# Kernel optimization log

Hardware: AMD Instinct MI355X
Metric: run time of the kernel (lower is better)

## Reference

```python
import jax, jax.numpy as jnp
import numpy as np

B, N, OUTERDIM, DIM, N_CLASSES = 2, 6000, 1024, 512, 2
HEADS, DIM_HEAD, INNER = 8, 64, 512
LANDMARKS, PINV_ITERS, KPAD = 256, 6, 16  # residual conv kernel 33 -> pad 16
SCALE = DIM_HEAD ** -0.5


def layer_norm(x, g, b, eps=1e-5):
    mu = x.mean(-1, keepdims=True)
    var = jnp.var(x, axis=-1, keepdims=True)
    return (x - mu) * jax.lax.rsqrt(var + eps) * g + b


def moore_penrose_pinv(x, iters=PINV_ITERS):
    # x: [b, h, m, m]
    abs_x = jnp.abs(x)
    col = abs_x.sum(-1)
    row = abs_x.sum(-2)
    z = jnp.swapaxes(x, -1, -2) / (jnp.max(col) * jnp.max(row))
    I = jnp.eye(x.shape[-1], dtype=x.dtype)
    for _ in range(iters):
        xz = x @ z
        z = 0.25 * z @ (13 * I - xz @ (15 * I - xz @ (7 * I - xz)))
    return z


def nystrom_attention(x, w_qkv, w_out, b_out, conv_w):
    b, n, _ = x.shape
    pad = (-n) % LANDMARKS
    xp = jnp.pad(x, ((0, 0), (pad, 0), (0, 0)))  # pad at FRONT, as in lucidrains impl
    npad = n + pad
    qkv = xp @ w_qkv.T  # [b, npad, 3*inner]
    q, k, v = [t.reshape(b, npad, HEADS, DIM_HEAD).transpose(0, 2, 1, 3)
               for t in jnp.split(qkv, 3, axis=-1)]
    q = q * SCALE
    l = npad // LANDMARKS  # tokens per landmark
    q_l = q.reshape(b, HEADS, LANDMARKS, l, DIM_HEAD).sum(3) / l
    k_l = k.reshape(b, HEADS, LANDMARKS, l, DIM_HEAD).sum(3) / l
    attn1 = jax.nn.softmax(jnp.einsum('bhid,bhjd->bhij', q, k_l), axis=-1)   # [b,h,npad,m]
    attn2 = jax.nn.softmax(jnp.einsum('bhid,bhjd->bhij', q_l, k_l), axis=-1)  # [b,h,m,m]
    attn3 = jax.nn.softmax(jnp.einsum('bhid,bhjd->bhij', q_l, k), axis=-1)    # [b,h,m,npad]
    out = (attn1 @ moore_penrose_pinv(attn2)) @ (attn3 @ v)  # [b,h,npad,d]
    # depthwise residual conv over sequence dim (per head), kernel (33,1)
    out = out + jax.lax.conv_general_dilated(
        v, conv_w, window_strides=(1, 1), padding=((KPAD, KPAD), (0, 0)),
        dimension_numbers=('NCHW', 'OIHW', 'NCHW'), feature_group_count=HEADS)
    out = out.transpose(0, 2, 1, 3).reshape(b, npad, INNER)
    out = out @ w_out.T + b_out
    return out[:, -n:]


def setup_inputs() -> dict:
    key = jax.random.key(0)
    ks = jax.random.split(key, 12)
    w = lambda k, shape: 0.02 * jax.random.normal(k, shape, dtype=jnp.float32)
    inp = {
        'data': jax.random.normal(ks[0], (B, N, OUTERDIM), dtype=jnp.float32),
        'w1': w(ks[1], (DIM, OUTERDIM)), 'b1': jnp.zeros((DIM,), jnp.float32),
        'cls_token': jax.random.normal(ks[2], (1, 1, DIM), dtype=jnp.float32),
        'ln1_g': jnp.ones((DIM,), jnp.float32), 'ln1_b': jnp.zeros((DIM,), jnp.float32),
        'qkv1_w': w(ks[3], (3 * INNER, DIM)),
        'out1_w': w(ks[4], (DIM, INNER)), 'out1_b': jnp.zeros((DIM,), jnp.float32),
        'conv1_w': w(ks[5], (HEADS, 1, 33, 1)),
        'ln2_g': jnp.ones((DIM,), jnp.float32), 'ln2_b': jnp.zeros((DIM,), jnp.float32),
        'qkv2_w': w(ks[6], (3 * INNER, DIM)),
        'out2_w': w(ks[7], (DIM, INNER)), 'out2_b': jnp.zeros((DIM,), jnp.float32),
        'conv2_w': w(ks[8], (HEADS, 1, 33, 1)),
        'lnf_g': jnp.ones((DIM,), jnp.float32), 'lnf_b': jnp.zeros((DIM,), jnp.float32),
        'w2': w(ks[9], (N_CLASSES, DIM)), 'b2': jnp.zeros((N_CLASSES,), jnp.float32),
    }
    return inp


def reference(data, w1, b1, cls_token, ln1_g, ln1_b, qkv1_w, out1_w, out1_b, conv1_w,
              ln2_g, ln2_b, qkv2_w, out2_w, out2_b, conv2_w, lnf_g, lnf_b, w2, b2):
    h = jax.nn.relu(data @ w1.T + b1)  # [B, N, DIM]
    H = h.shape[1]
    side = int(np.ceil(np.sqrt(H)))
    add = side * side - H
    h = jnp.concatenate([h, h[:, :add]], axis=1)  # square padding: 6084
    cls = jnp.broadcast_to(cls_token, (h.shape[0], 1, h.shape[2]))
    h = jnp.concatenate([cls, h], axis=1)  # +CLS: 6085
    h = h + nystrom_attention(layer_norm(h, ln1_g, ln1_b), qkv1_w, out1_w, out1_b, conv1_w)
    h = h + nystrom_attention(layer_norm(h, ln2_g, ln2_b), qkv2_w, out2_w, out2_b, conv2_w)
    h = layer_norm(h, lnf_g, lnf_b)[:, 0]
    logits = h @ w2.T + b2
    return logits
```

## Files before the change

kernel.cpp:

```cpp
#include <hip/hip_runtime.h>
#include <cstdint>
#include <cstddef>

namespace {

constexpr int DIMC  = 512;
constexpr int SEQ   = 6085;
constexpr int NPAD  = 6144;
constexpr int PADF  = 59;
constexpr int LMK   = 256;
constexpr int BHN   = 16;
constexpr int KSPL  = 16;
constexpr int MPADR = 6016;

typedef __attribute__((ext_vector_type(8))) short bf8_t;
typedef __attribute__((ext_vector_type(4))) float f4_t;

#define MFMA(a, b, c) __builtin_amdgcn_mfma_f32_16x16x32_bf16(a, b, c, 0, 0, 0)

#define SWZB(r, cu) (((((r) << 6) + ((cu) << 1))) ^ (((r) & 7) << 4))

#define GLDS16(gp, lp) __builtin_amdgcn_global_load_lds( \
    (const __attribute__((address_space(1))) void*)(gp), \
    (__attribute__((address_space(3))) void*)(lp), 16, 0, 0)

__device__ __forceinline__ ushort f2bf(float f) {
    union { float f; uint32_t u; } c{f};
    uint32_t u = c.u;
    return (ushort)((u + 0x7FFFu + ((u >> 16) & 1u)) >> 16);
}
__device__ __forceinline__ float bf2f(ushort u) {
    union { uint32_t u; float f; } c{(uint32_t)u << 16};
    return c.f;
}

__device__ __forceinline__ float waveSum(float v) {
#pragma unroll
    for (int o = 32; o > 0; o >>= 1) v += __shfl_xor(v, o, 64);
    return v;
}
__device__ __forceinline__ float waveMax(float v) {
#pragma unroll
    for (int o = 32; o > 0; o >>= 1) v = fmaxf(v, __shfl_xor(v, o, 64));
    return v;
}
__device__ __forceinline__ float blockSum256(float v, float* sm) {
    v = waveSum(v);
    __syncthreads();
    if ((threadIdx.x & 63) == 0) sm[threadIdx.x >> 6] = v;
    __syncthreads();
    return sm[0] + sm[1] + sm[2] + sm[3];
}
__device__ __forceinline__ float blockMax256(float v, float* sm) {
    v = waveMax(v);
    __syncthreads();
    if ((threadIdx.x & 63) == 0) sm[threadIdx.x >> 6] = v;
    __syncthreads();
    return fmaxf(fmaxf(sm[0], sm[1]), fmaxf(sm[2], sm[3]));
}
__device__ __forceinline__ float grpMax(float v) {
    v = fmaxf(v, __shfl_xor(v, 1, 64));
    v = fmaxf(v, __shfl_xor(v, 2, 64));
    v = fmaxf(v, __shfl_xor(v, 4, 64));
    v = fmaxf(v, __shfl_xor(v, 8, 64));
    return v;
}
__device__ __forceinline__ float grpSum(float v) {
    v += __shfl_xor(v, 1, 64);
    v += __shfl_xor(v, 2, 64);
    v += __shfl_xor(v, 4, 64);
    v += __shfl_xor(v, 8, 64);
    return v;
}

template<int EPI>
__global__ __launch_bounds__(256)
void gemm_bt(const ushort* __restrict__ A, const ushort* __restrict__ B,
             void* __restrict__ Cv, int M, int N, int K,
             int lda, int ldb, int ldc,
             long long sA, long long sB, long long sC,
             const float* __restrict__ bias, int relu,
             ushort* __restrict__ qp, ushort* __restrict__ kp, ushort* __restrict__ vp)
{
    __shared__ __align__(16) char As_s[128 * 128];
    __shared__ __align__(16) char Bs_s[128 * 128];
    const int gx = gridDim.x, gy = gridDim.y;
    const int total = gx * gy * gridDim.z;
    int flat = (blockIdx.z * gy + blockIdx.y) * gx + blockIdx.x;
    {
        int q = total >> 3, r = total & 7;
        int xcd = flat & 7, idx = flat >> 3;
        flat = (xcd < r ? xcd * (q + 1) : r * (q + 1) + (xcd - r) * q) + idx;
    }
    const int z = flat / (gx * gy);
    const int rem = flat - z * gx * gy;
    const int by = rem / gx, bx = rem - by * gx;

    const ushort* Ab = A + (size_t)z * sA;
    const ushort* Bb = B + (size_t)z * sB;
    const int row0 = by * 128, col0 = bx * 128;
    const int tid = threadIdx.x, wid = tid >> 6, lane = tid & 63;
    const int wr = wid >> 1, wc = wid & 1, lr = lane & 15, kg = lane >> 4;
    const int srow = lane >> 3, sq = lane & 7;
    f4_t acc[4][4] = {};
    for (int k0 = 0; k0 < K; k0 += 64) {
        __syncthreads();
#pragma unroll
        for (int i = 0; i < 4; ++i) {
            int r = wid * 32 + i * 8 + srow;
            int qs = sq ^ (r & 7);
            GLDS16(Ab + (size_t)(row0 + r) * lda + k0 + qs * 8,
                   As_s + (wid * 32 + i * 8) * 128);
        }
#pragma unroll
        for (int i = 0; i < 4; ++i) {
            int r = wid * 32 + i * 8 + srow;
            int qs = sq ^ (r & 7);
            GLDS16(Bb + (size_t)(col0 + r) * ldb + k0 + qs * 8,
                   Bs_s + (wid * 32 + i * 8) * 128);
        }
        asm volatile("s_waitcnt vmcnt(0)" ::: "memory");
        __syncthreads();
#pragma unroll
        for (int ks = 0; ks < 2; ++ks) {
            bf8_t af[4], bg[4];
#pragma unroll
            for (int mr = 0; mr < 4; ++mr) {
                int r = wr * 64 + mr * 16 + lr;
                af[mr] = *(const bf8_t*)(As_s + r * 128 + ((((ks << 2) | kg) ^ (r & 7)) << 4));
            }
#pragma unroll
            for (int nr = 0; nr < 4; ++nr) {
                int r = wc * 64 + nr * 16 + lr;
                bg[nr] = *(const bf8_t*)(Bs_s + r * 128 + ((((ks << 2) | kg) ^ (r & 7)) << 4));
            }
#pragma unroll
            for (int mr = 0; mr < 4; ++mr)
#pragma unroll
                for (int nr = 0; nr < 4; ++nr)
                    acc[mr][nr] = MFMA(af[mr], bg[nr], acc[mr][nr]);
        }
    }
#pragma unroll
    for (int mr = 0; mr < 4; ++mr) {
#pragma unroll
        for (int nr = 0; nr < 4; ++nr) {
#pragma unroll
            for (int r = 0; r < 4; ++r) {
                int gm = row0 + wr * 64 + mr * 16 + kg * 4 + r;
                int gn = col0 + wc * 64 + nr * 16 + lr;
                if (gm >= M || gn >= N) continue;
                float val = acc[mr][nr][r];
                if (EPI == 0) {
                    if (bias) val += bias[gn];
                    if (relu) val = fmaxf(val, 0.f);
                    ((float*)Cv)[(size_t)z * sC + (size_t)gm * ldc + gn] = val;
                } else if (EPI == 1) {
                    ((ushort*)Cv)[(size_t)z * sC + (size_t)gm * ldc + gn] = f2bf(val);
                } else if (EPI == 2) {
                    int b = (gm >= NPAD) ? 1 : 0;
                    int i = gm - b * NPAD;
                    int which = gn >> 9, hh = (gn >> 6) & 7, d = gn & 63;
                    int bh = b * 8 + hh;
                    if (which == 0)
                        qp[((size_t)bh * NPAD + i) * 64 + d] = f2bf(val * 0.125f);
                    else if (which == 1)
                        kp[((size_t)bh * NPAD + i) * 64 + d] = f2bf(val);
                    else
                        vp[((size_t)bh * NPAD + i) * 64 + d] = f2bf(val);
                } else {
                    int b = (gm >= NPAD) ? 1 : 0;
                    int i = gm - b * NPAD - PADF;
                    if (i >= 0) {
                        float* hp = (float*)Cv + ((size_t)(b * SEQ + i)) * DIMC + gn;
                        *hp += val + bias[gn];
                    }
                }
            }
        }
    }
}

__global__ void transpose_v(const ushort* __restrict__ in, ushort* __restrict__ out) {
    __shared__ ushort tile[32][33];
    int bh = blockIdx.z;
    int r0 = blockIdx.x * 32, c0 = blockIdx.y * 32;
    const ushort* ib = in + (size_t)bh * NPAD * 64;
    ushort* ob = out + (size_t)bh * 64 * NPAD;
    int x = threadIdx.x, y = threadIdx.y;
    for (int yy = y; yy < 32; yy += 8)
        tile[yy][x] = ib[(size_t)(r0 + yy) * 64 + c0 + x];
    __syncthreads();
    for (int yy = y; yy < 32; yy += 8)
        ob[(size_t)(c0 + yy) * NPAD + r0 + x] = tile[x][yy];
}

template<int OC, int OCT, int CTD>
__global__ __launch_bounds__(256)
void gemm_nt(const ushort* __restrict__ A, const ushort* __restrict__ Bt,
             ushort* __restrict__ C, ushort* __restrict__ CT,
             float alpha, float cd, int ldC, int ldCT,
             long long sA, long long sBt, long long sC, long long sCT)
{
    __shared__ __align__(16) char As_s[64 * 512];
    __shared__ __align__(16) char Bs_s[64 * 512];
    const int z = blockIdx.z;
    const int row0 = blockIdx.y * 64, col0 = blockIdx.x * 64;
    const int tid = threadIdx.x, wid = tid >> 6, lane = tid & 63;
    const int lr = lane & 15, kg = lane >> 4;
    const ushort* Ab = A + (size_t)z * sA;
    const ushort* Bb = Bt + (size_t)z * sBt;
    const int srow8 = lane >> 5;
    const int sch = lane & 31;
#pragma unroll
    for (int i = 0; i < 8; ++i) {
        int rb = i * 8 + wid * 2 + srow8;
        int qs = sch ^ (rb & 7);
        GLDS16(Ab + (size_t)(row0 + rb) * 256 + qs * 8,
               As_s + (i * 8 + wid * 2) * 512);
    }
#pragma unroll
    for (int i = 0; i < 8; ++i) {
        int rb = i * 8 + wid * 2 + srow8;
        int qs = sch ^ (rb & 7);
        GLDS16(Bb + (size_t)(col0 + rb) * 256 + qs * 8,
               Bs_s + (i * 8 + wid * 2) * 512);
    }
    asm volatile("s_waitcnt vmcnt(0)" ::: "memory");
    __syncthreads();
    f4_t acc[4] = {};
    const int arow = wid * 16 + lr;
#pragma unroll
    for (int ks = 0; ks < 8; ++ks) {
        bf8_t af = *(const bf8_t*)(As_s + arow * 512 + (((ks * 4 + kg) ^ (arow & 7)) << 4));
#pragma unroll
        for (int j = 0; j < 4; ++j) {
            int brow = j * 16 + lr;
            bf8_t bg = *(const bf8_t*)(Bs_s + brow * 512 + (((ks * 4 + kg) ^ (brow & 7)) << 4));
            acc[j] = MFMA(af, bg, acc[j]);
        }
    }
#pragma unroll
    for (int j = 0; j < 4; ++j) {
#pragma unroll
        for (int r = 0; r < 4; ++r) {
            int gm = row0 + wid * 16 + kg * 4 + r;
            int gn = col0 + j * 16 + lr;
            float val = alpha * acc[j][r];
            if (OC) C[(size_t)z * sC + (size_t)gm * ldC + gn] = f2bf(val);
            if (OCT) CT[(size_t)z * sCT + (size_t)gn * ldCT + gm] =
                f2bf(CTD ? (((gm == gn) ? cd : 0.f) - val) : val);
        }
    }
}

__global__ __launch_bounds__(256)
void row_stats(const ushort* __restrict__ S, float* __restrict__ lm,
               float* __restrict__ li)
{
    __shared__ float sm[4];
    const ushort* p = S + (size_t)blockIdx.x * NPAD;
    int t = threadIdx.x;
    float v[24];
    float mx = -1e30f;
#pragma unroll
    for (int j = 0; j < 24; ++j) { v[j] = bf2f(p[j * 256 + t]); mx = fmaxf(mx, v[j]); }
    float bm = blockMax256(mx, sm);
    float s = 0.f;
#pragma unroll
    for (int j = 0; j < 24; ++j) s += __expf(v[j] - bm);
    float bs = blockSum256(s, sm);
    if (t == 0) { lm[blockIdx.x] = bm; li[blockIdx.x] = 1.f / bs; }
}

__global__ __launch_bounds__(256)
void pv_splitk(const ushort* __restrict__ S, const ushort* __restrict__ vT,
               const float* __restrict__ lm, const float* __restrict__ li,
               float* __restrict__ o2p)
{
    __shared__ __align__(16) char As_s[128 * 64];
    __shared__ __align__(16) char Bs_s[64 * 64];
    __shared__ float smax[128], sinv[128];
    const int split = blockIdx.x, mt = blockIdx.y, bh = blockIdx.z;
    const int tid = threadIdx.x;
    const int wid = tid >> 6, lane = tid & 63;
    const int lr = lane & 15, kg = lane >> 4;
    const ushort* Sb = S + (size_t)bh * LMK * NPAD + (size_t)(mt * 128) * NPAD;
    const ushort* vTb = vT + (size_t)bh * 64 * NPAD;
    const int ks0 = split * (NPAD / KSPL);
    if (tid < 128) {
        smax[tid] = lm[bh * LMK + mt * 128 + tid];
        sinv[tid] = li[bh * LMK + mt * 128 + tid];
    }
    __syncthreads();
    f4_t acc[2][4] = {};
    for (int k0 = ks0; k0 < ks0 + NPAD / KSPL; k0 += 32) {
#pragma unroll
        for (int p = 0; p < 2; ++p) {
            int idx = p * 256 + tid;
            int m = idx >> 2, kc = (idx & 3) * 8;
            bf8_t raw = *(const bf8_t*)&Sb[(size_t)m * NPAD + k0 + kc];
            float mr = smax[m], iv = sinv[m];
            bf8_t o;
#pragma unroll
            for (int j = 0; j < 8; ++j)
                o[j] = (short)f2bf(__expf(bf2f((ushort)raw[j]) - mr) * iv);
            *(bf8_t*)(As_s + SWZB(m, kc)) = o;
        }
        {
            int n = tid >> 2, kc = (tid & 3) * 8;
            *(bf8_t*)(Bs_s + SWZB(n, kc)) = *(const bf8_t*)&vTb[(size_t)n * NPAD + k0 + kc];
        }
        __syncthreads();
        bf8_t af[2], bg[4];
#pragma unroll
        for (int i = 0; i < 2; ++i)
            af[i] = *(const bf8_t*)(As_s + SWZB(wid * 32 + i * 16 + lr, kg * 8));
#pragma unroll
        for (int j = 0; j < 4; ++j)
            bg[j] = *(const bf8_t*)(Bs_s + SWZB(j * 16 + lr, kg * 8));
#pragma unroll
        for (int i = 0; i < 2; ++i)
#pragma unroll
            for (int j = 0; j < 4; ++j)
                acc[i][j] = MFMA(af[i], bg[j], acc[i][j]);
        __syncthreads();
    }
#pragma unroll
    for (int i = 0; i < 2; ++i)
#pragma unroll
        for (int j = 0; j < 4; ++j)
#pragma unroll
            for (int r = 0; r < 4; ++r) {
                int gm = mt * 128 + wid * 32 + i * 16 + kg * 4 + r;
                int gn = j * 16 + lr;
                o2p[((size_t)(split * BHN + bh) * LMK + gm) * 64 + gn] = acc[i][j][r];
            }
}

__global__ void reduce_o2(const float* __restrict__ o2p, ushort* __restrict__ o2t) {
    int idx = blockIdx.x * 256 + threadIdx.x;
    int bh = idx >> 14, m = (idx >> 6) & 255, d = idx & 63;
    float s = 0.f;
#pragma unroll
    for (int sp = 0; sp < KSPL; ++sp)
        s += o2p[((size_t)(sp * BHN + bh) << 14) + (m << 6) + d];
    o2t[((size_t)bh * 64 + d) * 256 + m] = f2bf(s);
}

__global__ __launch_bounds__(256)
void attn1_fused(const ushort* __restrict__ q, const ushort* __restrict__ kl,
                 const ushort* __restrict__ Wt, ushort* __restrict__ ot)
{
    __shared__ __align__(16) char P_s[64 * 512];
    const int mt = blockIdx.x;
    const int bh = blockIdx.y;
    const int b = bh >> 3, hh = bh & 7;
    const int tid = threadIdx.x, wid = tid >> 6, lane = tid & 63;
    const int lr = lane & 15, kg = lane >> 4;
    const int row0 = mt * 64, rowb = wid * 16;
    const ushort* qb  = q  + (size_t)bh * NPAD * 64;
    const ushort* klb = kl + (size_t)bh * LMK * 64;
    const ushort* Wtb = Wt + (size_t)bh * 128 * 256;

    f4_t acc[16];
#pragma unroll
    for (int nf = 0; nf < 16; ++nf) acc[nf] = (f4_t){0.f, 0.f, 0.f, 0.f};
#pragma unroll
    for (int ks = 0; ks < 2; ++ks) {
        bf8_t af = *(const bf8_t*)&qb[(size_t)(row0 + rowb + lr) * 64 + ks * 32 + kg * 8];
#pragma unroll
        for (int nf = 0; nf < 16; ++nf) {
            bf8_t bg = *(const bf8_t*)&klb[(size_t)(nf * 16 + lr) * 64 + ks * 32 + kg * 8];
            acc[nf] = MFMA(af, bg, acc[nf]);
        }
    }
    float inv_s[4];
    {
        float mx[4] = {-3.0e38f, -3.0e38f, -3.0e38f, -3.0e38f};
#pragma unroll
        for (int nf = 0; nf < 16; ++nf)
#pragma unroll
            for (int r = 0; r < 4; ++r) mx[r] = fmaxf(mx[r], acc[nf][r]);
#pragma unroll
        for (int r = 0; r < 4; ++r) mx[r] = grpMax(mx[r]);
        float sum[4] = {0.f, 0.f, 0.f, 0.f};
        const int rb2 = rowb + kg * 4;
        const int cc2 = (lr & 7) * 2, chi = lr >> 3;
#pragma unroll
        for (int nf = 0; nf < 16; ++nf)
#pragma unroll
            for (int r = 0; r < 4; ++r) {
                float e = __expf(acc[nf][r] - mx[r]);
                sum[r] += e;
                int row = rb2 + r;
                int chunk = (2 * nf + chi) ^ (row & 7);
                *(ushort*)(P_s + row * 512 + chunk * 16 + cc2) = f2bf(e);
            }
#pragma unroll
        for (int r = 0; r < 4; ++r) inv_s[r] = 1.f / grpSum(sum[r]);
    }
    f4_t acc2[4] = {};
#pragma unroll
    for (int kt = 0; kt < 8; ++kt) {
        int row = rowb + lr;
        int chunk = (kt * 4 + kg) ^ (row & 7);
        bf8_t af2 = *(const bf8_t*)(P_s + row * 512 + chunk * 16);
#pragma unroll
        for (int nf = 0; nf < 4; ++nf) {
            bf8_t bg = *(const bf8_t*)&Wtb[(size_t)(nf * 16 + lr) * 256 + kt * 32 + kg * 8];
            acc2[nf] = MFMA(af2, bg, acc2[nf]);
        }
    }
#pragma unroll
    for (int nf = 0; nf < 4; ++nf)
#pragma unroll
        for (int r = 0; r < 4; ++r) {
            int gm = row0 + rowb + kg * 4 + r;
            int gn = nf * 16 + lr;
            ot[((size_t)(b * NPAD + gm)) * DIMC + hh * 64 + gn] = f2bf(acc2[nf][r] * inv_s[r]);
        }
}

__global__ void cvt_bf16(const float* __restrict__ in, ushort* __restrict__ out, int n8) {
    int i = blockIdx.x * 256 + threadIdx.x;
    if (i >= n8) return;
    float4 a = ((const float4*)in)[i * 2], b = ((const float4*)in)[i * 2 + 1];
    ushort4 lo = { f2bf(a.x), f2bf(a.y), f2bf(a.z), f2bf(a.w) };
    ushort4 hi = { f2bf(b.x), f2bf(b.y), f2bf(b.z), f2bf(b.w) };
    ((ushort4*)out)[i * 2] = lo;
    ((ushort4*)out)[i * 2 + 1] = hi;
}

__global__ void extend_h(float* __restrict__ h, const float* __restrict__ cls) {
    int b = blockIdx.y, bx = blockIdx.x;
    float* hb = h + (size_t)b * SEQ * DIMC;
    for (int c = threadIdx.x; c < DIMC; c += 256) {
        if (bx == 0) hb[c] = cls[c];
        else hb[(size_t)(6000 + bx) * DIMC + c] = hb[(size_t)bx * DIMC + c];
    }
}

__global__ void zero_xp_pad(ushort* __restrict__ xp) {
    int e = blockIdx.x * 256 + threadIdx.x;
    int b = e / (PADF * DIMC);
    int rest = e - b * (PADF * DIMC);
    xp[(size_t)b * NPAD * DIMC + rest] = 0;
}

__global__ __launch_bounds__(128)
void ln_to_xp(const float* __restrict__ h, const float* __restrict__ g,
              const float* __restrict__ bb, ushort* __restrict__ xp)
{
    __shared__ float sm[2];
    int r = blockIdx.x;
    int b = r / SEQ, i = r - b * SEQ;
    int t = threadIdx.x;
    const float4* row = (const float4*)(h + (size_t)r * DIMC);
    float4 x = row[t];
    float s  = x.x + x.y + x.z + x.w;
    float sq = x.x * x.x + x.y * x.y + x.z * x.z + x.w * x.w;
    s = waveSum(s);
    sq = waveSum(sq);
    int w = t >> 6;
    if ((t & 63) == 0) sm[w] = s;
    __syncthreads();
    float S = sm[0] + sm[1];
    __syncthreads();
    if ((t & 63) == 0) sm[w] = sq;
    __syncthreads();
    float SQ = sm[0] + sm[1];
    float mu = S * (1.f / DIMC);
    float var = SQ * (1.f / DIMC) - mu * mu;
    float rs = rsqrtf(var + 1e-5f);
    float4 gg = ((const float4*)g)[t];
    float4 bv = ((const float4*)bb)[t];
    ushort4 o;
    o.x = f2bf((x.x - mu) * rs * gg.x + bv.x);
    o.y = f2bf((x.y - mu) * rs * gg.y + bv.y);
    o.z = f2bf((x.z - mu) * rs * gg.z + bv.z);
    o.w = f2bf((x.w - mu) * rs * gg.w + bv.w);
    ((ushort4*)(xp + ((size_t)b * NPAD + PADF + i) * DIMC))[t] = o;
}

__global__ void landmark_mean(const ushort* __restrict__ in, ushort* __restrict__ out) {
    int m = blockIdx.x, bh = blockIdx.y, d = threadIdx.x;
    const ushort* p = in + ((size_t)bh * NPAD + (size_t)m * (NPAD / LMK)) * 64 + d;
    float s = 0.f;
#pragma unroll
    for (int j = 0; j < NPAD / LMK; ++j) s += bf2f(p[(size_t)j * 64]);
    out[((size_t)bh * LMK + m) * 64 + d] = f2bf(s * (1.f / (NPAD / LMK)));
}

__global__ __launch_bounds__(256)
void softmax_bf256(ushort* __restrict__ S) {
    __shared__ float sm[4];
    ushort* p = S + (size_t)blockIdx.x * 256;
    int t = threadIdx.x;
    float v = bf2f(p[t]);
    float bm = blockMax256(v, sm);
    float e = __expf(v - bm);
    float bs = blockSum256(e, sm);
    p[t] = f2bf(e / bs);
}

__global__ __launch_bounds__(256)
void colsum_max(const ushort* __restrict__ X, float* __restrict__ scal) {
    __shared__ float sm[4];
    int bh = blockIdx.x, t = threadIdx.x;
    const ushort* Xb = X + ((size_t)bh << 16);
    float s = 0.f;
#pragma unroll 8
    for (int i = 0; i < 256; ++i) s += bf2f(Xb[(size_t)i * 256 + t]);
    float m = blockMax256(s, sm);
    if (t == 0) atomicMax((unsigned int*)scal, __float_as_uint(m));
}

__global__ void init_z(const ushort* __restrict__ X, const float* __restrict__ scal,
                       ushort* __restrict__ Z, ushort* __restrict__ Zt) {
    size_t e = (size_t)blockIdx.x * 256 + threadIdx.x;
    int c = (int)(e & 255);
    int r = (int)((e >> 8) & 255);
    size_t bh = e >> 16;
    float inv = 1.f / scal[0];
    Z[e]  = f2bf(bf2f(X[(bh << 16) + (size_t)c * 256 + r]) * inv);
    Zt[e] = f2bf(bf2f(X[e]) * inv);
}

__global__ __launch_bounds__(256)
void conv_add(const ushort* __restrict__ v, const float* __restrict__ cw,
              ushort* __restrict__ ot)
{
    __shared__ float w[33];
    __shared__ ushort vt[96][64];
    int bh = blockIdx.y;
    int b = bh >> 3, hh = bh & 7;
    int i0 = blockIdx.x * 64;
    int t = threadIdx.x;
    if (t < 33) w[t] = cw[hh * 33 + t];
    const ushort* vb = v + (size_t)bh * NPAD * 64;
    int d = t & 63;
    for (int rr = t >> 6; rr < 96; rr += 4) {
        int j = i0 - 16 + rr;
        vt[rr][d] = (j >= 0 && j < NPAD) ? vb[(size_t)j * 64 + d] : (ushort)0;
    }
    __syncthreads();
    for (int ii = t >> 6; ii < 64; ii += 4) {
        float acc = 0.f;
#pragma unroll
        for (int kk = 0; kk < 33; ++kk) acc += w[kk] * bf2f(vt[ii + kk][d]);
        size_t off = ((size_t)(b * NPAD + i0 + ii)) * DIMC + hh * 64 + d;
        ot[off] = f2bf(bf2f(ot[off]) + acc);
    }
}

__global__ __launch_bounds__(256)
void final_head(const float* __restrict__ h, const float* __restrict__ g,
                const float* __restrict__ bb, const float* __restrict__ w2,
                const float* __restrict__ b2, float* __restrict__ out)
{
    __shared__ float row[DIMC];
    __shared__ float sm[4];
    int b = blockIdx.x;
    int t = threadIdx.x;
    const float* x = h + (size_t)b * SEQ * DIMC;
    float v0 = x[t], v1 = x[t + 256];
    float S = blockSum256(v0 + v1, sm);
    float SQ = blockSum256(v0 * v0 + v1 * v1, sm);
    float mu = S * (1.f / DIMC);
    float rs = rsqrtf(SQ * (1.f / DIMC) - mu * mu + 1e-5f);
    row[t] = (v0 - mu) * rs * g[t] + bb[t];
    row[t + 256] = (v1 - mu) * rs * g[t + 256] + bb[t + 256];
    __syncthreads();
    if (t < 64) {
        float a0 = 0.f, a1 = 0.f;
        for (int idx = t; idx < DIMC; idx += 64) {
            a0 += row[idx] * w2[idx];
            a1 += row[idx] * w2[DIMC + idx];
        }
        a0 = waveSum(a0);
        a1 = waveSum(a1);
        if (t == 0) {
            out[b * 2 + 0] = a0 + b2[0];
            out[b * 2 + 1] = a1 + b2[1];
        }
    }
}

void bt(int epi, const ushort* A, const ushort* B, void* C, int M, int N, int K,
        int lda, int ldb, int ldc, long long sA, long long sB, long long sC, int batch,
        const float* bias, int relu, ushort* qp, ushort* kp, ushort* vp, hipStream_t s)
{
    dim3 g((N + 127) / 128, (M + 127) / 128, batch), blk(256);
    switch (epi) {
    case 0: gemm_bt<0><<<g, blk, 0, s>>>(A, B, C, M, N, K, lda, ldb, ldc, sA, sB, sC, bias, relu, qp, kp, vp); break;
    case 1: gemm_bt<1><<<g, blk, 0, s>>>(A, B, C, M, N, K, lda, ldb, ldc, sA, sB, sC, bias, relu, qp, kp, vp); break;
    case 2: gemm_bt<2><<<g, blk, 0, s>>>(A, B, C, M, N, K, lda, ldb, ldc, sA, sB, sC, bias, relu, qp, kp, vp); break;
    default: gemm_bt<3><<<g, blk, 0, s>>>(A, B, C, M, N, K, lda, ldb, ldc, sA, sB, sC, bias, relu, qp, kp, vp); break;
    }
}

void nt(int mode, const ushort* A, const ushort* Bt, ushort* C, ushort* CT,
        float alpha, float cd, int M, int N, int ldC, int ldCT,
        long long sA, long long sBt, long long sC, long long sCT, hipStream_t s)
{
    dim3 g(N / 64, M / 64, BHN), blk(256);
    switch (mode) {
    case 0: gemm_nt<1, 1, 1><<<g, blk, 0, s>>>(A, Bt, C, CT, alpha, cd, ldC, ldCT, sA, sBt, sC, sCT); break;
    case 1: gemm_nt<0, 1, 1><<<g, blk, 0, s>>>(A, Bt, C, CT, alpha, cd, ldC, ldCT, sA, sBt, sC, sCT); break;
    case 2: gemm_nt<1, 1, 0><<<g, blk, 0, s>>>(A, Bt, C, CT, alpha, cd, ldC, ldCT, sA, sBt, sC, sCT); break;
    default: gemm_nt<0, 1, 0><<<g, blk, 0, s>>>(A, Bt, C, CT, alpha, cd, ldC, ldCT, sA, sBt, sC, sCT); break;
    }
}

struct WS {
    float *h, *scal, *o2p, *lm, *li;
    ushort *xp, *q, *k, *v, *vT, *ql, *kl;
    ushort *datab, *w1b, *qkvwb1, *qkvwb2, *outwb1, *outwb2;
    ushort *X, *Y, *TAt, *TBt, *Z0, *Z0t, *Z1, *Z1t;
    ushort *o2t, *Wt, *S, *ot;
};

void nystrom_layer(float* h, const float* lng, const float* lnb,
                   const ushort* qkvwb, const ushort* outwb, const float* outb,
                   const float* convw, const WS& w, hipStream_t s)
{
    const long long SM = (long long)LMK * LMK;
    zero_xp_pad<<<(2 * PADF * DIMC) / 256, 256, 0, s>>>(w.xp);
    ln_to_xp<<<2 * SEQ, 128, 0, s>>>(h, lng, lnb, w.xp);
    bt(2, w.xp, qkvwb, nullptr, 2 * NPAD, 3 * DIMC, DIMC, DIMC, DIMC, 0,
       0, 0, 0, 1, nullptr, 0, w.q, w.k, w.v, s);
    transpose_v<<<dim3(NPAD / 32, 2, BHN), dim3(32, 8), 0, s>>>(w.v, w.vT);
    landmark_mean<<<dim3(LMK, BHN), 64, 0, s>>>(w.q, w.ql);
    landmark_mean<<<dim3(LMK, BHN), 64, 0, s>>>(w.k, w.kl);
    bt(1, w.ql, w.kl, w.X, LMK, LMK, 64, 64, 64, LMK,
       (long long)LMK * 64, (long long)LMK * 64, SM, BHN,
       nullptr, 0, nullptr, nullptr, nullptr, s);
    softmax_bf256<<<BHN * LMK, 256, 0, s>>>(w.X);
    hipMemsetAsync(w.scal, 0, 8, s);
    colsum_max<<<BHN, 256, 0, s>>>(w.X, w.scal);
    init_z<<<(BHN * LMK * LMK) / 256, 256, 0, s>>>(w.X, w.scal, w.Z0, w.Z0t);
    ushort *Zc = w.Z0, *Zct = w.Z0t, *Zn = w.Z1, *Znt = w.Z1t;
    for (int it = 0; it < 6; ++it) {
        nt(0, w.X, Zct, w.Y, w.TAt, 1.f, 7.f, LMK, LMK, 256, 256, SM, SM, SM, SM, s);
        nt(1, w.Y, w.TAt, nullptr, w.TBt, 1.f, 15.f, LMK, LMK, 256, 256, SM, SM, 0, SM, s);
        nt(1, w.Y, w.TBt, nullptr, w.TAt, 1.f, 13.f, LMK, LMK, 256, 256, SM, SM, 0, SM, s);
        nt(2, Zc, w.TAt, Zn, Znt, 0.25f, 0.f, LMK, LMK, 256, 256, SM, SM, SM, SM, s);
        ushort* t;
        t = Zc; Zc = Zn; Zn = t;
        t = Zct; Zct = Znt; Znt = t;
    }
    bt(1, w.ql, w.k, w.S, LMK, NPAD, 64, 64, 64, NPAD,
       (long long)LMK * 64, (long long)NPAD * 64, (long long)LMK * NPAD, BHN,
       nullptr, 0, nullptr, nullptr, nullptr, s);
    row_stats<<<BHN * LMK, 256, 0, s>>>(w.S, w.lm, w.li);
    pv_splitk<<<dim3(KSPL, 2, BHN), 256, 0, s>>>(w.S, w.vT, w.lm, w.li, w.o2p);
    reduce_o2<<<BHN * LMK * 64 / 256, 256, 0, s>>>(w.o2p, w.o2t);
    nt(3, Zc, w.o2t, nullptr, w.Wt, 1.f, 0.f, LMK, 64, 256, 256,
       SM, 64 * 256, 0, 128 * 256, s);
    attn1_fused<<<dim3(NPAD / 64, BHN), 256, 0, s>>>(w.q, w.kl, w.Wt, w.ot);
    conv_add<<<dim3(NPAD / 64, BHN), 256, 0, s>>>(w.v, convw, w.ot);
    bt(3, w.ot, outwb, h, 2 * NPAD, DIMC, DIMC, DIMC, DIMC, 0,
       0, 0, 0, 1, outb, 0, nullptr, nullptr, nullptr, s);
}

}

extern "C" void kernel_launch(void* const* d_in, const int* in_sizes, int n_in,
                              void* d_out, int out_size, void* d_ws, size_t ws_size,
                              hipStream_t stream)
{
    (void)in_sizes; (void)n_in; (void)out_size;
    const float* data  = (const float*)d_in[0];
    const float* w1    = (const float*)d_in[1];
    const float* b1    = (const float*)d_in[2];
    const float* cls   = (const float*)d_in[3];
    const float* ln1g  = (const float*)d_in[4];
    const float* ln1b  = (const float*)d_in[5];
    const float* qkv1w = (const float*)d_in[6];
    const float* out1w = (const float*)d_in[7];
    const float* out1b = (const float*)d_in[8];
    const float* conv1 = (const float*)d_in[9];
    const float* ln2g  = (const float*)d_in[10];
    const float* ln2b  = (const float*)d_in[11];
    const float* qkv2w = (const float*)d_in[12];
    const float* out2w = (const float*)d_in[13];
    const float* out2b = (const float*)d_in[14];
    const float* conv2 = (const float*)d_in[15];
    const float* lnfg  = (const float*)d_in[16];
    const float* lnfb  = (const float*)d_in[17];
    const float* w2    = (const float*)d_in[18];
    const float* b2    = (const float*)d_in[19];
    float* out = (float*)d_out;

    if (ws_size < 209473792ull) return;
    char* p = (char*)d_ws;
    auto alloc = [&](size_t bytes) { char* r = p; p += (bytes + 255) & ~(size_t)255; return r; };
    WS w;
    w.h     = (float*)alloc((size_t)2 * SEQ * DIMC * 4);
    w.xp    = (ushort*)alloc((size_t)2 * NPAD * DIMC * 2);
    w.q     = (ushort*)alloc((size_t)BHN * NPAD * 64 * 2);
    w.k     = (ushort*)alloc((size_t)BHN * NPAD * 64 * 2);
    w.v     = (ushort*)alloc((size_t)BHN * NPAD * 64 * 2);
    w.vT    = (ushort*)alloc((size_t)BHN * 64 * NPAD * 2);
    w.ql    = (ushort*)alloc((size_t)BHN * LMK * 64 * 2);
    w.kl    = (ushort*)alloc((size_t)BHN * LMK * 64 * 2);
    w.scal  = (float*)alloc(256);
    w.lm    = (float*)alloc((size_t)BHN * LMK * 4);
    w.li    = (float*)alloc((size_t)BHN * LMK * 4);
    w.datab = (ushort*)alloc((size_t)2 * MPADR * 1024 * 2);
    w.w1b   = (ushort*)alloc((size_t)512 * 1024 * 2);
    w.qkvwb1= (ushort*)alloc((size_t)1536 * 512 * 2);
    w.qkvwb2= (ushort*)alloc((size_t)1536 * 512 * 2);
    w.outwb1= (ushort*)alloc((size_t)512 * 512 * 2);
    w.outwb2= (ushort*)alloc((size_t)512 * 512 * 2);
    w.X     = (ushort*)alloc((size_t)BHN * LMK * LMK * 2);
    w.Y     = (ushort*)alloc((size_t)BHN * LMK * LMK * 2);
    w.TAt   = (ushort*)alloc((size_t)BHN * LMK * LMK * 2);
    w.TBt   = (ushort*)alloc((size_t)BHN * LMK * LMK * 2);
    w.Z0    = (ushort*)alloc((size_t)BHN * LMK * LMK * 2);
    w.Z0t   = (ushort*)alloc((size_t)BHN * LMK * LMK * 2);
    w.Z1    = (ushort*)alloc((size_t)BHN * LMK * LMK * 2);
    w.Z1t   = (ushort*)alloc((size_t)BHN * LMK * LMK * 2);
    w.o2p   = (float*)alloc((size_t)KSPL * BHN * LMK * 64 * 4);
    w.o2t   = (ushort*)alloc((size_t)BHN * 64 * 256 * 2);
    w.Wt    = (ushort*)alloc((size_t)BHN * 128 * 256 * 2);
    w.S     = (ushort*)alloc((size_t)BHN * LMK * NPAD * 2);
    w.ot    = w.k;

    for (int b = 0; b < 2; ++b)
        cvt_bf16<<<3000, 256, 0, stream>>>(data + (size_t)b * 6000 * 1024,
                                           w.datab + (size_t)b * MPADR * 1024, 768000);
    cvt_bf16<<<256, 256, 0, stream>>>(w1, w.w1b, 65536);
    cvt_bf16<<<384, 256, 0, stream>>>(qkv1w, w.qkvwb1, 98304);
    cvt_bf16<<<384, 256, 0, stream>>>(qkv2w, w.qkvwb2, 98304);
    cvt_bf16<<<128, 256, 0, stream>>>(out1w, w.outwb1, 32768);
    cvt_bf16<<<128, 256, 0, stream>>>(out2w, w.outwb2, 32768);

    bt(0, w.datab, w.w1b, w.h + DIMC, 6000, DIMC, 1024, 1024, 1024, DIMC,
       (long long)MPADR * 1024, 0, (long long)SEQ * DIMC, 2, b1, 1,
       nullptr, nullptr, nullptr, stream);
    extend_h<<<dim3(85, 2), 256, 0, stream>>>(w.h, cls);

    nystrom_layer(w.h, ln1g, ln1b, w.qkvwb1, w.outwb1, out1b, conv1, w, stream);
    nystrom_layer(w.h, ln2g, ln2b, w.qkvwb2, w.outwb2, out2b, conv2, w, stream);

    final_head<<<2, 256, 0, stream>>>(w.h, lnfg, lnfb, w2, b2, out);
}
```

Before: 880.1 us.

## Fuse attn3 scores, softmax and PV into a flash-style split-K kernel

Replaces the separate q_l·k^T GEMM, the materialized S score matrix, the row_stats pass and the pv_splitk kernel with one flash-style kernel. Each block computes scores for 128 keys, applies a local softmax and multiplies by V. It writes partial outputs with per-split max and sum, and reduce_o2 rescales and combines them. This drops the write and two reads of a large bf16 score matrix plus two launches. In exchange it adds a 48-way partial buffer and a heavier reduction that reads 48 partials per element.

```diff
diff --git a/kernel.cpp b/kernel.cpp
--- a/kernel.cpp
+++ b/kernel.cpp
@@ -10,7 +10,7 @@
 constexpr int PADF  = 59;
 constexpr int LMK   = 256;
 constexpr int BHN   = 16;
-constexpr int KSPL  = 16;
+constexpr int KSP3  = 48;
 constexpr int MPADR = 6016;
 
 typedef __attribute__((ext_vector_type(8))) short bf8_t;
@@ -255,97 +255,115 @@
 }
 
 __global__ __launch_bounds__(256)
-void row_stats(const ushort* __restrict__ S, float* __restrict__ lm,
-               float* __restrict__ li)
-{
-    __shared__ float sm[4];
-    const ushort* p = S + (size_t)blockIdx.x * NPAD;
-    int t = threadIdx.x;
-    float v[24];
-    float mx = -1e30f;
-#pragma unroll
-    for (int j = 0; j < 24; ++j) { v[j] = bf2f(p[j * 256 + t]); mx = fmaxf(mx, v[j]); }
-    float bm = blockMax256(mx, sm);
-    float s = 0.f;
-#pragma unroll
-    for (int j = 0; j < 24; ++j) s += __expf(v[j] - bm);
-    float bs = blockSum256(s, sm);
-    if (t == 0) { lm[blockIdx.x] = bm; li[blockIdx.x] = 1.f / bs; }
-}
-
-__global__ __launch_bounds__(256)
-void pv_splitk(const ushort* __restrict__ S, const ushort* __restrict__ vT,
-               const float* __restrict__ lm, const float* __restrict__ li,
-               float* __restrict__ o2p)
-{
-    __shared__ __align__(16) char As_s[128 * 64];
-    __shared__ __align__(16) char Bs_s[64 * 64];
-    __shared__ float smax[128], sinv[128];
+void pv_flash(const ushort* __restrict__ ql, const ushort* __restrict__ k,
+              const ushort* __restrict__ vT, float* __restrict__ o2p,
+              float* __restrict__ lmb, float* __restrict__ lsb)
+{
+    __shared__ __align__(16) char P_s[128 * 256];
     const int split = blockIdx.x, mt = blockIdx.y, bh = blockIdx.z;
-    const int tid = threadIdx.x;
-    const int wid = tid >> 6, lane = tid & 63;
+    const int tid = threadIdx.x, wid = tid >> 6, lane = tid & 63;
     const int lr = lane & 15, kg = lane >> 4;
-    const ushort* Sb = S + (size_t)bh * LMK * NPAD + (size_t)(mt * 128) * NPAD;
+    const int rowb = wid * 32;
+    const ushort* qlb = ql + ((size_t)bh * LMK + mt * 128) * 64;
+    const ushort* kb  = k  + (size_t)bh * NPAD * 64;
     const ushort* vTb = vT + (size_t)bh * 64 * NPAD;
-    const int ks0 = split * (NPAD / KSPL);
-    if (tid < 128) {
-        smax[tid] = lm[bh * LMK + mt * 128 + tid];
-        sinv[tid] = li[bh * LMK + mt * 128 + tid];
-    }
-    __syncthreads();
-    f4_t acc[2][4] = {};
-    for (int k0 = ks0; k0 < ks0 + NPAD / KSPL; k0 += 32) {
-#pragma unroll
-        for (int p = 0; p < 2; ++p) {
-            int idx = p * 256 + tid;
-            int m = idx >> 2, kc = (idx & 3) * 8;
-            bf8_t raw = *(const bf8_t*)&Sb[(size_t)m * NPAD + k0 + kc];
-            float mr = smax[m], iv = sinv[m];
-            bf8_t o;
-#pragma unroll
-            for (int j = 0; j < 8; ++j)
-                o[j] = (short)f2bf(__expf(bf2f((ushort)raw[j]) - mr) * iv);
-            *(bf8_t*)(As_s + SWZB(m, kc)) = o;
-        }
-        {
-            int n = tid >> 2, kc = (tid & 3) * 8;
-            *(bf8_t*)(Bs_s + SWZB(n, kc)) = *(const bf8_t*)&vTb[(size_t)n * NPAD + k0 + kc];
-        }
-        __syncthreads();
-        bf8_t af[2], bg[4];
-#pragma unroll
-        for (int i = 0; i < 2; ++i)
-            af[i] = *(const bf8_t*)(As_s + SWZB(wid * 32 + i * 16 + lr, kg * 8));
-#pragma unroll
-        for (int j = 0; j < 4; ++j)
-            bg[j] = *(const bf8_t*)(Bs_s + SWZB(j * 16 + lr, kg * 8));
-#pragma unroll
-        for (int i = 0; i < 2; ++i)
-#pragma unroll
-            for (int j = 0; j < 4; ++j)
-                acc[i][j] = MFMA(af[i], bg[j], acc[i][j]);
-        __syncthreads();
-    }
-#pragma unroll
-    for (int i = 0; i < 2; ++i)
-#pragma unroll
-        for (int j = 0; j < 4; ++j)
+    const int kvb = split * 128;
+
+    f4_t sacc[2][8] = {};
+#pragma unroll
+    for (int ks = 0; ks < 2; ++ks) {
+        bf8_t af[2];
+#pragma unroll
+        for (int mf = 0; mf < 2; ++mf)
+            af[mf] = *(const bf8_t*)&qlb[(size_t)(rowb + mf * 16 + lr) * 64 + ks * 32 + kg * 8];
+#pragma unroll
+        for (int nf = 0; nf < 8; ++nf) {
+            bf8_t bg = *(const bf8_t*)&kb[(size_t)(kvb + nf * 16 + lr) * 64 + ks * 32 + kg * 8];
+            sacc[0][nf] = MFMA(af[0], bg, sacc[0][nf]);
+            sacc[1][nf] = MFMA(af[1], bg, sacc[1][nf]);
+        }
+    }
+    float mloc[2][4], lloc[2][4];
+#pragma unroll
+    for (int mf = 0; mf < 2; ++mf) {
+        float tmax[4] = {-3.0e38f, -3.0e38f, -3.0e38f, -3.0e38f};
+#pragma unroll
+        for (int nf = 0; nf < 8; ++nf)
+#pragma unroll
+            for (int r = 0; r < 4; ++r) tmax[r] = fmaxf(tmax[r], sacc[mf][nf][r]);
+#pragma unroll
+        for (int r = 0; r < 4; ++r) { tmax[r] = grpMax(tmax[r]); mloc[mf][r] = tmax[r]; }
+        float lsum[4] = {0.f, 0.f, 0.f, 0.f};
+        const int rb2 = rowb + mf * 16 + kg * 4;
+        const int cc2 = (lr & 7) * 2, chi = lr >> 3;
+#pragma unroll
+        for (int nf = 0; nf < 8; ++nf)
 #pragma unroll
             for (int r = 0; r < 4; ++r) {
-                int gm = mt * 128 + wid * 32 + i * 16 + kg * 4 + r;
-                int gn = j * 16 + lr;
-                o2p[((size_t)(split * BHN + bh) * LMK + gm) * 64 + gn] = acc[i][j][r];
+                float e = __expf(sacc[mf][nf][r] - tmax[r]);
+                lsum[r] += e;
+                int row = rb2 + r;
+                int chunk = (2 * nf + chi) ^ (row & 7);
+                *(ushort*)(P_s + row * 256 + chunk * 16 + cc2) = f2bf(e);
             }
-}
-
-__global__ void reduce_o2(const float* __restrict__ o2p, ushort* __restrict__ o2t) {
+#pragma unroll
+        for (int r = 0; r < 4; ++r) lloc[mf][r] = grpSum(lsum[r]);
+    }
+    f4_t acco[2][4] = {};
+#pragma unroll
+    for (int kt2 = 0; kt2 < 4; ++kt2) {
+        bf8_t af2[2];
+#pragma unroll
+        for (int mf = 0; mf < 2; ++mf) {
+            int row = rowb + mf * 16 + lr;
+            int chunk = (kt2 * 4 + kg) ^ (row & 7);
+            af2[mf] = *(const bf8_t*)(P_s + row * 256 + chunk * 16);
+        }
+#pragma unroll
+        for (int nf2 = 0; nf2 < 4; ++nf2) {
+            bf8_t bg = *(const bf8_t*)&vTb[(size_t)(nf2 * 16 + lr) * NPAD + kvb + kt2 * 32 + kg * 8];
+            acco[0][nf2] = MFMA(af2[0], bg, acco[0][nf2]);
+            acco[1][nf2] = MFMA(af2[1], bg, acco[1][nf2]);
+        }
+    }
+#pragma unroll
+    for (int mf = 0; mf < 2; ++mf)
+#pragma unroll
+        for (int nf2 = 0; nf2 < 4; ++nf2)
+#pragma unroll
+            for (int r = 0; r < 4; ++r) {
+                int gm = mt * 128 + rowb + mf * 16 + kg * 4 + r;
+                o2p[((size_t)(split * BHN + bh) * LMK + gm) * 64 + nf2 * 16 + lr] = acco[mf][nf2][r];
+            }
+    if (lr == 0) {
+#pragma unroll
+        for (int mf = 0; mf < 2; ++mf)
+#pragma unroll
+            for (int r = 0; r < 4; ++r) {
+                int gm = mt * 128 + rowb + mf * 16 + kg * 4 + r;
+                lmb[(size_t)(split * BHN + bh) * LMK + gm] = mloc[mf][r];
+                lsb[(size_t)(split * BHN + bh) * LMK + gm] = lloc[mf][r];
+            }
+    }
+}
+
+__global__ void reduce_o2(const float* __restrict__ o2p, const float* __restrict__ lmb,
+                          const float* __restrict__ lsb, ushort* __restrict__ o2t)
+{
     int idx = blockIdx.x * 256 + threadIdx.x;
     int bh = idx >> 14, m = (idx >> 6) & 255, d = idx & 63;
-    float s = 0.f;
-#pragma unroll
-    for (int sp = 0; sp < KSPL; ++sp)
-        s += o2p[((size_t)(sp * BHN + bh) << 14) + (m << 6) + d];
-    o2t[((size_t)bh * 64 + d) * 256 + m] = f2bf(s);
+    float gm = -3.0e38f;
+#pragma unroll 8
+    for (int s = 0; s < KSP3; ++s)
+        gm = fmaxf(gm, lmb[(size_t)(s * BHN + bh) * LMK + m]);
+    float num = 0.f, den = 0.f;
+#pragma unroll 4
+    for (int s = 0; s < KSP3; ++s) {
+        float wgt = __expf(lmb[(size_t)(s * BHN + bh) * LMK + m] - gm);
+        num += wgt * o2p[((size_t)(s * BHN + bh) << 14) + (m << 6) + d];
+        den += wgt * lsb[(size_t)(s * BHN + bh) * LMK + m];
+    }
+    o2t[((size_t)bh * 64 + d) * 256 + m] = f2bf(num / den);
 }
 
 __global__ __launch_bounds__(256)
@@ -614,11 +632,11 @@
 }
 
 struct WS {
-    float *h, *scal, *o2p, *lm, *li;
+    float *h, *scal, *o2p, *lmb, *lsb;
     ushort *xp, *q, *k, *v, *vT, *ql, *kl;
     ushort *datab, *w1b, *qkvwb1, *qkvwb2, *outwb1, *outwb2;
     ushort *X, *Y, *TAt, *TBt, *Z0, *Z0t, *Z1, *Z1t;
-    ushort *o2t, *Wt, *S, *ot;
+    ushort *o2t, *Wt, *ot;
 };
 
 void nystrom_layer(float* h, const float* lng, const float* lnb,
@@ -650,12 +668,8 @@
         t = Zc; Zc = Zn; Zn = t;
         t = Zct; Zct = Znt; Znt = t;
     }
-    bt(1, w.ql, w.k, w.S, LMK, NPAD, 64, 64, 64, NPAD,
-       (long long)LMK * 64, (long long)NPAD * 64, (long long)LMK * NPAD, BHN,
-       nullptr, 0, nullptr, nullptr, nullptr, s);
-    row_stats<<<BHN * LMK, 256, 0, s>>>(w.S, w.lm, w.li);
-    pv_splitk<<<dim3(KSPL, 2, BHN), 256, 0, s>>>(w.S, w.vT, w.lm, w.li, w.o2p);
-    reduce_o2<<<BHN * LMK * 64 / 256, 256, 0, s>>>(w.o2p, w.o2t);
+    pv_flash<<<dim3(KSP3, 2, BHN), 256, 0, s>>>(w.ql, w.k, w.vT, w.o2p, w.lmb, w.lsb);
+    reduce_o2<<<BHN * LMK * 64 / 256, 256, 0, s>>>(w.o2p, w.lmb, w.lsb, w.o2t);
     nt(3, Zc, w.o2t, nullptr, w.Wt, 1.f, 0.f, LMK, 64, 256, 256,
        SM, 64 * 256, 0, 128 * 256, s);
     attn1_fused<<<dim3(NPAD / 64, BHN), 256, 0, s>>>(w.q, w.kl, w.Wt, w.ot);
@@ -706,8 +720,8 @@
     w.ql    = (ushort*)alloc((size_t)BHN * LMK * 64 * 2);
     w.kl    = (ushort*)alloc((size_t)BHN * LMK * 64 * 2);
     w.scal  = (float*)alloc(256);
-    w.lm    = (float*)alloc((size_t)BHN * LMK * 4);
-    w.li    = (float*)alloc((size_t)BHN * LMK * 4);
+    w.lmb   = (float*)alloc((size_t)KSP3 * BHN * LMK * 4);
+    w.lsb   = (float*)alloc((size_t)KSP3 * BHN * LMK * 4);
     w.datab = (ushort*)alloc((size_t)2 * MPADR * 1024 * 2);
     w.w1b   = (ushort*)alloc((size_t)512 * 1024 * 2);
     w.qkvwb1= (ushort*)alloc((size_t)1536 * 512 * 2);
@@ -722,10 +736,9 @@
     w.Z0t   = (ushort*)alloc((size_t)BHN * LMK * LMK * 2);
     w.Z1    = (ushort*)alloc((size_t)BHN * LMK * LMK * 2);
     w.Z1t   = (ushort*)alloc((size_t)BHN * LMK * LMK * 2);
-    w.o2p   = (float*)alloc((size_t)KSPL * BHN * LMK * 64 * 4);
+    w.o2p   = (float*)alloc((size_t)KSP3 * BHN * LMK * 64 * 4);
     w.o2t   = (ushort*)alloc((size_t)BHN * 64 * 256 * 2);
     w.Wt    = (ushort*)alloc((size_t)BHN * 128 * 256 * 2);
-    w.S     = (ushort*)alloc((size_t)BHN * LMK * NPAD * 2);
     w.ot    = w.k;
 
     for (int b = 0; b < 2; ++b)
```

Result: slower. 899.7 us (+2.2%).
